# Optimization experiments

Hardware: AMD Instinct MI355X
Metric: run time of the kernel (lower is better)

## Reference

```python
import jax, jax.numpy as jnp
import numpy as np

EPS = 1e-6
POSE_W, DEPTH_W, POINTS_W, NORMAL_W = 1.0, 1.0, 1.0, 0.1
DEPTH_MIN = 1e-6


def mat_to_quat(M):
    # pytorch3d-style robust rotation-matrix -> quaternion (w,x,y,z)
    m00, m01, m02 = M[..., 0, 0], M[..., 0, 1], M[..., 0, 2]
    m10, m11, m12 = M[..., 1, 0], M[..., 1, 1], M[..., 1, 2]
    m20, m21, m22 = M[..., 2, 0], M[..., 2, 1], M[..., 2, 2]
    q_abs = jnp.sqrt(jnp.maximum(jnp.stack([
        1.0 + m00 + m11 + m22,
        1.0 + m00 - m11 - m22,
        1.0 - m00 + m11 - m22,
        1.0 - m00 - m11 + m22], axis=-1), 0.0))
    cand = jnp.stack([
        jnp.stack([q_abs[..., 0] ** 2, m21 - m12, m02 - m20, m10 - m01], -1),
        jnp.stack([m21 - m12, q_abs[..., 1] ** 2, m10 + m01, m02 + m20], -1),
        jnp.stack([m02 - m20, m10 + m01, q_abs[..., 2] ** 2, m12 + m21], -1),
        jnp.stack([m10 - m01, m20 + m02, m21 + m12, q_abs[..., 3] ** 2], -1),
    ], axis=-2)  # [...,4,4]
    cand = cand / (2.0 * jnp.maximum(q_abs[..., None], 0.1))
    best = jnp.argmax(q_abs, axis=-1)
    quat = jnp.take_along_axis(cand, best[..., None, None], axis=-2)[..., 0, :]
    return jnp.where(quat[..., 0:1] < 0, -quat, quat)


def pose_encoding(extri, intr, H, W):
    # extri [B,S,3,4] -> [B,S,9] = absT(3) + quat(4) + fov_h,fov_w
    T = extri[..., :3, 3]
    quat = mat_to_quat(extri[..., :3, :3])
    fov_h = 2.0 * jnp.arctan((H / 2.0) / intr[..., 1, 1])
    fov_w = 2.0 * jnp.arctan((W / 2.0) / intr[..., 0, 0])
    return jnp.concatenate([T, quat, fov_h[..., None], fov_w[..., None]], axis=-1)


def align_depth_scale(dp, dg, vm):
    # batched masked-median scale; dp detached by caller. Returns (aligned_gt, scales[B,S])
    B, S, H, W = dg.shape
    dpf, dgf = dp.reshape(B, S, H * W), dg.reshape(B, S, H * W)
    m = vm.reshape(B, S, H * W)
    m2 = m & jnp.isfinite(dpf) & (dpf > EPS)
    ratio = dpf / jnp.maximum(dgf, EPS)
    fm = m2 & jnp.isfinite(ratio)
    msum = m2.sum(-1)
    fcnt = fm.sum(-1)
    r = jnp.sort(jnp.where(fm, ratio, jnp.inf), axis=-1)
    idx = jnp.maximum((fcnt - 1) // 2, 0)  # torch lower median
    med = jnp.take_along_axis(r, idx[..., None], axis=-1)[..., 0]
    scale = jnp.clip(med, 1e-3, 1e3)
    scale = jnp.where((msum < 16) | (fcnt == 0), jnp.ones_like(scale), scale)
    return dg * scale[..., None, None], scale


def _cam_grid(depth, intr):
    B, S, H, W = depth.shape
    ys, xs = jnp.meshgrid(jnp.arange(H, dtype=depth.dtype),
                          jnp.arange(W, dtype=depth.dtype), indexing='ij')
    fx = intr[..., 0, 0][..., None, None]
    fy = intr[..., 1, 1][..., None, None]
    cx = intr[..., 0, 2][..., None, None]
    cy = intr[..., 1, 2][..., None, None]
    x = (xs - cx) / jnp.maximum(fx, EPS) * depth
    y = (ys - cy) / jnp.maximum(fy, EPS) * depth
    return jnp.stack([x, y, depth], axis=-1)  # [B,S,H,W,3]


def depth_to_normals(depth, intr):
    pts = _cam_grid(depth, intr)
    fx_diff = pts[..., 1:-1, 2:, :] - pts[..., 1:-1, :-2, :]
    fy_diff = pts[..., 2:, 1:-1, :] - pts[..., :-2, 1:-1, :]
    core = jnp.cross(fy_diff, fx_diff)
    core = core / jnp.maximum(jnp.linalg.norm(core, axis=-1, keepdims=True), EPS)
    return jnp.zeros_like(pts).at[..., 1:-1, 1:-1, :].set(core)


def depth_to_world_points(depth, intr, pose):
    cam_pts = _cam_grid(depth, intr)
    rot = pose[..., :3, :3]
    trans = pose[..., :3, 3]
    return jnp.einsum('bsij,bshwj->bshwi', rot, cam_pts) + trans[..., None, None, :]


def masked_l1(pred, target, mask):
    mask = mask.astype(pred.dtype)
    return ((pred - target) * mask).__abs__().sum() / jnp.maximum(mask.sum(), 1.0)


def masked_cosine_loss(pred, target, mask):
    pred = pred / jnp.maximum(jnp.linalg.norm(pred, axis=-1, keepdims=True), EPS)
    target = target / jnp.maximum(jnp.linalg.norm(target, axis=-1, keepdims=True), EPS)
    cos = jnp.clip((pred * target).sum(-1), -1.0, 1.0)
    m = mask.astype(cos.dtype)
    return ((1.0 - cos) * m).sum() / jnp.maximum(m.sum(), 1.0)


def smooth_l1(pred, target):
    d = jnp.abs(pred - target)
    return jnp.mean(jnp.where(d < 1.0, 0.5 * d * d, d - 0.5))


def supervised_loss(depth_pred, points_pred, pose_pred, depth_gt, intrinsics,
                    pose_matrix_gt, valid_mask):
    B, S, H, W = depth_gt.shape
    vm = valid_mask & jnp.isfinite(depth_gt) & (depth_gt > DEPTH_MIN)
    depth_gt_aligned, scales = align_depth_scale(
        jax.lax.stop_gradient(depth_pred), depth_gt, vm)
    points_gt = depth_to_world_points(depth_gt_aligned, intrinsics, pose_matrix_gt)
    points_mask = jnp.broadcast_to(vm[..., None], points_gt.shape)
    # normal mask: zero-out 1-pixel border
    border = jnp.zeros((H, W), dtype=bool).at[1:-1, 1:-1].set(True)
    normal_mask = vm & border
    pred_normals = depth_to_normals(depth_pred, intrinsics)
    gt_normals = depth_to_normals(depth_gt, intrinsics)
    normal_loss = masked_cosine_loss(pred_normals, gt_normals, normal_mask)
    pose_gt = pose_encoding(pose_matrix_gt[..., :3, :], intrinsics, H, W)
    pose_gt = pose_gt.at[..., :3].multiply(scales[..., None])
    depth_loss = masked_l1(depth_pred, depth_gt_aligned, vm)
    points_loss = masked_l1(points_pred, points_gt, points_mask)
    pose_loss = smooth_l1(pose_pred, pose_gt)
    return (POSE_W * pose_loss + DEPTH_W * depth_loss
            + POINTS_W * points_loss + NORMAL_W * normal_loss)


def setup_inputs() -> dict:
    key = jax.random.key(0)
    ks = jax.random.split(key, 7)
    B, S, H, W = 4, 8, 384, 512
    depth_gt = jax.random.uniform(ks[0], (B, S, H, W), minval=0.5, maxval=10.0)
    depth_pred = depth_gt * jax.random.uniform(ks[1], (B, S, H, W), minval=0.8, maxval=1.2)
    points_pred = jax.random.normal(ks[2], (B, S, H, W, 3))
    pose_pred = 0.1 * jax.random.normal(ks[3], (B, S, 9))
    intr = jnp.broadcast_to(jnp.array([[500.0, 0.0, W / 2.0],
                                       [0.0, 500.0, H / 2.0],
                                       [0.0, 0.0, 1.0]], jnp.float32), (B, S, 3, 3))
    q, _ = jnp.linalg.qr(jax.random.normal(ks[4], (B, S, 3, 3)))
    R = q * jnp.sign(jnp.linalg.det(q))[..., None, None]  # det=+1
    t = jax.random.normal(ks[5], (B, S, 3))
    top = jnp.concatenate([R, t[..., None]], axis=-1)
    bottom = jnp.broadcast_to(jnp.array([0.0, 0.0, 0.0, 1.0], jnp.float32), (B, S, 1, 4))
    pose_matrix_gt = jnp.concatenate([top, bottom], axis=-2)
    valid_mask = jax.random.uniform(ks[6], (B, S, H, W)) > 0.05
    return {"depth_pred": depth_pred, "points_pred": points_pred,
            "pose_pred": pose_pred, "depth_gt": depth_gt,
            "intrinsics": intr, "pose_matrix_gt": pose_matrix_gt,
            "valid_mask": valid_mask}


def reference(depth_pred, points_pred, pose_pred, depth_gt, intrinsics,
              pose_matrix_gt, valid_mask):
    return supervised_loss(depth_pred, points_pred, pose_pred, depth_gt,
                           intrinsics, pose_matrix_gt, valid_mask)
```

## Files before the change

### kernel.cpp

```cpp
#include <hip/hip_runtime.h>
#include <stdint.h>

#define H_ 384
#define W_ 512
#define HW_ (H_ * W_)
#define NIMG 32
#define EPSF 1e-6f
#define HBLK 16
#define HTHR 512
#define PXB (HW_ / HBLK)
#define CITER (PXB / (HTHR * 4))
#define MBLK 96
#define NPARTS (MBLK * NIMG)
#define SENT 0xFFFFFFFFu

#define OFF_MSUM   0
#define OFF_FCNT   32
#define OFF_KREM1  64
#define OFF_PREF1  96
#define OFF_POSE   128
#define OFF_PMF    160
#define OFF_PART   1184
#define OFF_PHA    16544
#define OFF_PHB    (OFF_PHA + NIMG*HBLK*2048)

__device__ __forceinline__ bool finitef(float x) {
    return ((__float_as_uint(x) >> 23) & 0xFFu) != 0xFFu;
}

__global__ __launch_bounds__(HTHR) void hist0_k(
    const float* __restrict__ dp, const float* __restrict__ dg,
    const uint8_t* __restrict__ vmask, uint32_t* __restrict__ ws)
{
    __shared__ uint32_t lh[2048];
    __shared__ int sm[8], sf[8];
    const int img = blockIdx.y, blk = blockIdx.x, t = threadIdx.x;
    for (int b = t; b < 2048; b += HTHR) lh[b] = 0;
    __syncthreads();

    const size_t base = (size_t)img * HW_;
    const float* dpi = dp + base;
    const float* dgi = dg + base;
    const uint8_t* mi = vmask + base;

    int m2c = 0, fmc = 0;

    for (int c = 0; c < CITER; ++c) {
        const int pix = blk * PXB + c * (HTHR * 4) + t * 4;
        const float4 v_dp = *reinterpret_cast<const float4*>(dpi + pix);
        const float4 v_dg = *reinterpret_cast<const float4*>(dgi + pix);
        const uchar4 v_m  = *reinterpret_cast<const uchar4*>(mi + pix);
        const float dpa[4] = {v_dp.x, v_dp.y, v_dp.z, v_dp.w};
        const float dga[4] = {v_dg.x, v_dg.y, v_dg.z, v_dg.w};
        const uint8_t ma[4] = {v_m.x, v_m.y, v_m.z, v_m.w};
        int bins[4]; bool fms[4];
#pragma unroll
        for (int e = 0; e < 4; ++e) {
            const float dgv = dga[e], dpv = dpa[e];
            const bool vm = ma[e] && finitef(dgv) && (dgv > 1e-6f);
            const bool m2 = vm && finitef(dpv) && (dpv > EPSF);
            const float ratio = dpv / fmaxf(dgv, EPSF);
            const bool fm = m2 && finitef(ratio);
            m2c += (int)m2; fmc += (int)fm;
            const uint32_t key = fm ? __float_as_uint(ratio) : SENT;
            bins[e] = (int)(key >> 21);
            fms[e] = fm;
        }

#pragma unroll
        for (int e = 0; e < 4; ++e) {
            const bool fm = fms[e];
            const int bin = bins[e];
            unsigned long long todo = __ballot(fm);
            while (todo) {
                const int lead = (int)__ffsll(todo) - 1;
                const int lbin = __shfl(bin, lead);
                const unsigned long long same = __ballot(fm && (bin == lbin));
                if ((t & 63) == lead)
                    atomicAdd(&lh[lbin], (uint32_t)__popcll(same));
                todo &= ~same;
            }
        }
    }

    for (int o = 32; o > 0; o >>= 1) { m2c += __shfl_down(m2c, o); fmc += __shfl_down(fmc, o); }
    if ((t & 63) == 0) { sm[t >> 6] = m2c; sf[t >> 6] = fmc; }
    __syncthreads();
    if (t == 0) {
        int M = 0, F = 0;
        for (int w = 0; w < 8; ++w) { M += sm[w]; F += sf[w]; }
        int* pmf = (int*)(ws + OFF_PMF) + (img * HBLK + blk) * 2;
        pmf[0] = M; pmf[1] = F;
    }

    uint32_t* phb = ws + OFF_PHA + (size_t)(img * HBLK + blk) * 2048;
    for (int b = t; b < 2048; b += HTHR) phb[b] = lh[b];
}

__global__ __launch_bounds__(HTHR) void histp1_k(
    const float* __restrict__ dp, const float* __restrict__ dg,
    const uint8_t* __restrict__ vmask, uint32_t* __restrict__ ws)
{
    __shared__ uint32_t lh[256];
    __shared__ uint32_t wsum[8];
    __shared__ int s_bin, s_krem, s_msum, s_fcnt;
    const int img = blockIdx.y, blk = blockIdx.x, t = threadIdx.x;

    const uint32_t* pin = ws + OFF_PHA + (size_t)img * HBLK * 2048;
    uint32_t local[4];
#pragma unroll
    for (int c = 0; c < 4; ++c) local[c] = 0;
    for (int b = 0; b < HBLK; ++b) {
        const uint32_t* row = pin + b * 2048 + t * 4;
#pragma unroll
        for (int c = 0; c < 4; ++c) local[c] += row[c];
    }
    const uint32_t cs = local[0] + local[1] + local[2] + local[3];

    uint32_t v = cs;
#pragma unroll
    for (int o = 1; o < 64; o <<= 1) {
        const uint32_t u = __shfl_up(v, o);
        if ((t & 63) >= o) v += u;
    }
    if ((t & 63) == 63) wsum[t >> 6] = v;
    if (t == 0) {
        s_bin = 0; s_krem = 0;
        const int* pmf = (const int*)(ws + OFF_PMF) + img * HBLK * 2;
        int M = 0, F = 0;
        for (int b = 0; b < HBLK; ++b) { M += pmf[2 * b]; F += pmf[2 * b + 1]; }
        s_msum = M; s_fcnt = F;
    }
    __syncthreads();
    uint32_t woff = 0;
    for (int w = 0; w < (t >> 6); ++w) woff += wsum[w];
    const uint32_t incl = woff + v;
    const uint32_t excl = incl - cs;

    const uint32_t k = (uint32_t)max((s_fcnt - 1) / 2, 0);
    if (k >= excl && k < incl) {
        uint32_t cum = excl;
#pragma unroll
        for (int c = 0; c < 4; ++c) {
            if (cum + local[c] > k) { s_bin = t * 4 + c; s_krem = (int)(k - cum); break; }
            cum += local[c];
        }
    }
    __syncthreads();
    if (t == 0 && blk == 0) {
        ((int*)(ws + OFF_MSUM))[img] = s_msum;
        ((int*)(ws + OFF_FCNT))[img] = s_fcnt;
        (ws + OFF_PREF1)[img] = (uint32_t)s_bin << 21;
        ((int*)(ws + OFF_KREM1))[img] = s_krem;
    }
    const uint32_t pm = (uint32_t)s_bin;

    if (t < 256) lh[t] = 0;
    __syncthreads();

    const size_t base = (size_t)img * HW_;
    for (int c = 0; c < CITER; ++c) {
        const int pix = blk * PXB + c * (HTHR * 4) + t * 4;
        const float4 v_dp = *reinterpret_cast<const float4*>(dp + base + pix);
        const float4 v_dg = *reinterpret_cast<const float4*>(dg + base + pix);
        const uchar4 v_m  = *reinterpret_cast<const uchar4*>(vmask + base + pix);
        const float dpa[4] = {v_dp.x, v_dp.y, v_dp.z, v_dp.w};
        const float dga[4] = {v_dg.x, v_dg.y, v_dg.z, v_dg.w};
        const uint8_t ma[4] = {v_m.x, v_m.y, v_m.z, v_m.w};
#pragma unroll
        for (int e = 0; e < 4; ++e) {
            const float dgv = dga[e], dpv = dpa[e];
            const bool vm = ma[e] && finitef(dgv) && (dgv > 1e-6f);
            const bool m2 = vm && finitef(dpv) && (dpv > EPSF);
            const float ratio = dpv / fmaxf(dgv, EPSF);
            const bool fm = m2 && finitef(ratio);
            const uint32_t key = fm ? __float_as_uint(ratio) : SENT;
            if ((key >> 21) == pm)
                atomicAdd(&lh[(key >> 13) & 255u], 1u);
        }
    }
    __syncthreads();

    uint32_t* pout = ws + OFF_PHB + (size_t)(img * HBLK + blk) * 256;
    if (t < 256) pout[t] = lh[t];
}

__global__ __launch_bounds__(256) void main_loss(
    const float* __restrict__ dp, const float* __restrict__ dg,
    const uint8_t* __restrict__ vmask, const float* __restrict__ pts_pred,
    const float* __restrict__ intr, const float* __restrict__ posegt,
    const float* __restrict__ posepred, uint32_t* __restrict__ ws)
{
    const int img = blockIdx.y;
    const int t = threadIdx.x;

    __shared__ uint32_t wsum[4];
    __shared__ int s_bin;
    __shared__ float sP[17];
    {
        const uint32_t* ph = ws + OFF_PHB + (size_t)img * HBLK * 256;
        uint32_t cs = 0;
        for (int b = 0; b < HBLK; ++b) cs += ph[b * 256 + t];
        uint32_t v = cs;
#pragma unroll
        for (int o = 1; o < 64; o <<= 1) {
            const uint32_t u = __shfl_up(v, o);
            if ((t & 63) >= o) v += u;
        }
        if ((t & 63) == 63) wsum[t >> 6] = v;
        if (t == 0) s_bin = 0;
        __syncthreads();
        uint32_t woff = 0;
        for (int w = 0; w < (t >> 6); ++w) woff += wsum[w];
        const uint32_t incl = woff + v;
        const uint32_t excl = incl - cs;
        const uint32_t k = (uint32_t)((const int*)(ws + OFF_KREM1))[img];
        if (k >= excl && k < incl) s_bin = t;
        __syncthreads();
    }
    if (t == 0) {
        const uint32_t med_u = (ws + OFF_PREF1)[img] | ((uint32_t)s_bin << 13) | 4096u;
        const float med = __uint_as_float(med_u);
        float sc_ = fminf(fmaxf(med, 0.001f), 1000.0f);
        const int fcnt = ((const int*)(ws + OFF_FCNT))[img];
        const int msum = ((const int*)(ws + OFF_MSUM))[img];
        if (msum < 16 || fcnt == 0) sc_ = 1.0f;

        const float* p = posegt + img * 16;
        sP[0] = p[0]; sP[1] = p[1]; sP[2] = p[2];  sP[9]  = p[3];
        sP[3] = p[4]; sP[4] = p[5]; sP[5] = p[6];  sP[10] = p[7];
        sP[6] = p[8]; sP[7] = p[9]; sP[8] = p[10]; sP[11] = p[11];
        sP[12] = intr[img * 9 + 0]; sP[13] = intr[img * 9 + 4];
        sP[14] = intr[img * 9 + 2]; sP[15] = intr[img * 9 + 5];
        sP[16] = sc_;

        if (blockIdx.x == 0) {
            const float m00 = p[0], m01 = p[1], m02 = p[2], tx = p[3];
            const float m10 = p[4], m11 = p[5], m12 = p[6], ty = p[7];
            const float m20 = p[8], m21 = p[9], m22 = p[10], tz = p[11];
            float qa[4];
            qa[0] = sqrtf(fmaxf(1.0f + m00 + m11 + m22, 0.0f));
            qa[1] = sqrtf(fmaxf(1.0f + m00 - m11 - m22, 0.0f));
            qa[2] = sqrtf(fmaxf(1.0f - m00 + m11 - m22, 0.0f));
            qa[3] = sqrtf(fmaxf(1.0f - m00 - m11 + m22, 0.0f));
            int best = 0; float bv = qa[0];
            for (int i2 = 1; i2 < 4; ++i2) if (qa[i2] > bv) { bv = qa[i2]; best = i2; }
            float c0, c1, c2, c3;
            if (best == 0)      { c0 = qa[0]*qa[0]; c1 = m21 - m12;   c2 = m02 - m20;   c3 = m10 - m01; }
            else if (best == 1) { c0 = m21 - m12;   c1 = qa[1]*qa[1]; c2 = m10 + m01;   c3 = m02 + m20; }
            else if (best == 2) { c0 = m02 - m20;   c1 = m10 + m01;   c2 = qa[2]*qa[2]; c3 = m12 + m21; }
            else                { c0 = m10 - m01;   c1 = m20 + m02;   c2 = m21 + m12;   c3 = qa[3]*qa[3]; }
            const float denom = 2.0f * fmaxf(qa[best], 0.1f);
            float q0 = c0 / denom, q1 = c1 / denom, q2 = c2 / denom, q3 = c3 / denom;
            if (q0 < 0.0f) { q0 = -q0; q1 = -q1; q2 = -q2; q3 = -q3; }
            const float fx = sP[12], fy = sP[13];
            const float fovh = 2.0f * atanf((H_ * 0.5f) / fy);
            const float fovw = 2.0f * atanf((W_ * 0.5f) / fx);
            const float pg[9] = {tx * sc_, ty * sc_, tz * sc_, q0, q1, q2, q3, fovh, fovw};
            const float* ppred = posepred + img * 9;
            float s = 0.0f;
            for (int i2 = 0; i2 < 9; ++i2) {
                const float d = fabsf(ppred[i2] - pg[i2]);
                s += (d < 1.0f) ? 0.5f * d * d : d - 0.5f;
            }
            ((float*)(ws + OFF_POSE))[img] = s;
        }
    }
    __syncthreads();
    const float R00 = sP[0], R01 = sP[1], R02 = sP[2];
    const float R10 = sP[3], R11 = sP[4], R12 = sP[5];
    const float R20 = sP[6], R21 = sP[7], R22 = sP[8];
    const float T0 = sP[9], T1 = sP[10], T2 = sP[11];
    const float inv_fx = 1.0f / fmaxf(sP[12], EPSF);
    const float inv_fy = 1.0f / fmaxf(sP[13], EPSF);
    const float cx = sP[14], cy = sP[15];
    const float sc = sP[16];

    const size_t base = (size_t)img * HW_;
    const int pix0 = (blockIdx.x * 256 + t) * 8;
    const int i = pix0 >> 9;
    const int j0 = pix0 & 511;
    const float* dpi = dp + base;
    const float* dgi = dg + base;

    const float4 dpC0 = *reinterpret_cast<const float4*>(dpi + pix0);
    const float4 dpC1 = *reinterpret_cast<const float4*>(dpi + pix0 + 4);
    const float4 dgC0 = *reinterpret_cast<const float4*>(dgi + pix0);
    const float4 dgC1 = *reinterpret_cast<const float4*>(dgi + pix0 + 4);
    const uchar4 m0 = *reinterpret_cast<const uchar4*>(vmask + base + pix0);
    const uchar4 m1 = *reinterpret_cast<const uchar4*>(vmask + base + pix0 + 4);
    const float4 pp0 = *reinterpret_cast<const float4*>(pts_pred + (base + pix0) * 3);
    const float4 pp1 = *reinterpret_cast<const float4*>(pts_pred + (base + pix0) * 3 + 4);
    const float4 pp2 = *reinterpret_cast<const float4*>(pts_pred + (base + pix0) * 3 + 8);
    const float4 pp3 = *reinterpret_cast<const float4*>(pts_pred + (base + pix0) * 3 + 12);
    const float4 pp4 = *reinterpret_cast<const float4*>(pts_pred + (base + pix0) * 3 + 16);
    const float4 pp5 = *reinterpret_cast<const float4*>(pts_pred + (base + pix0) * 3 + 20);

    const int im = (i > 0) ? i - 1 : 0;
    const int ip = (i < H_ - 1) ? i + 1 : i;
    const int jme = (j0 > 0) ? j0 - 1 : 0;
    const int jpe = (j0 + 8 < W_) ? j0 + 8 : W_ - 1;
    const float4 dpU0 = *reinterpret_cast<const float4*>(dpi + im * W_ + j0);
    const float4 dpU1 = *reinterpret_cast<const float4*>(dpi + im * W_ + j0 + 4);
    const float4 dpD0 = *reinterpret_cast<const float4*>(dpi + ip * W_ + j0);
    const float4 dpD1 = *reinterpret_cast<const float4*>(dpi + ip * W_ + j0 + 4);
    const float4 dgU0 = *reinterpret_cast<const float4*>(dgi + im * W_ + j0);
    const float4 dgU1 = *reinterpret_cast<const float4*>(dgi + im * W_ + j0 + 4);
    const float4 dgD0 = *reinterpret_cast<const float4*>(dgi + ip * W_ + j0);
    const float4 dgD1 = *reinterpret_cast<const float4*>(dgi + ip * W_ + j0 + 4);
    const float dpLe = dpi[i * W_ + jme], dpRe = dpi[i * W_ + jpe];
    const float dgLe = dgi[i * W_ + jme], dgRe = dgi[i * W_ + jpe];

    const float ppv[24] = {pp0.x, pp0.y, pp0.z, pp0.w, pp1.x, pp1.y, pp1.z, pp1.w,
                           pp2.x, pp2.y, pp2.z, pp2.w, pp3.x, pp3.y, pp3.z, pp3.w,
                           pp4.x, pp4.y, pp4.z, pp4.w, pp5.x, pp5.y, pp5.z, pp5.w};
    const float dpa[8] = {dpC0.x, dpC0.y, dpC0.z, dpC0.w, dpC1.x, dpC1.y, dpC1.z, dpC1.w};
    const float dga[8] = {dgC0.x, dgC0.y, dgC0.z, dgC0.w, dgC1.x, dgC1.y, dgC1.z, dgC1.w};
    const float dpUa[8] = {dpU0.x, dpU0.y, dpU0.z, dpU0.w, dpU1.x, dpU1.y, dpU1.z, dpU1.w};
    const float dpDa[8] = {dpD0.x, dpD0.y, dpD0.z, dpD0.w, dpD1.x, dpD1.y, dpD1.z, dpD1.w};
    const float dgUa[8] = {dgU0.x, dgU0.y, dgU0.z, dgU0.w, dgU1.x, dgU1.y, dgU1.z, dgU1.w};
    const float dgDa[8] = {dgD0.x, dgD0.y, dgD0.z, dgD0.w, dgD1.x, dgD1.y, dgD1.z, dgD1.w};
    const uint8_t ma[8] = {m0.x, m0.y, m0.z, m0.w, m1.x, m1.y, m1.z, m1.w};

    const float ay = ((float)i - cy) * inv_fy;
    const bool row_int = (i >= 1) && (i <= H_ - 2);

    float dsum = 0.0f, psum = 0.0f, nsum = 0.0f;
    float vcnt = 0.0f, ncnt = 0.0f;

#pragma unroll
    for (int e = 0; e < 8; ++e) {
        const int j = j0 + e;
        const float dgv = dga[e], dpv = dpa[e];
        const bool vm = ma[e] && finitef(dgv) && (dgv > 1e-6f);
        const bool nm = vm && row_int && (j >= 1) && (j <= W_ - 2);
        vcnt += vm ? 1.0f : 0.0f;
        ncnt += nm ? 1.0f : 0.0f;

        const float dal = dgv * sc;
        dsum += vm ? fabsf(dpv - dal) : 0.0f;
        const float ax = ((float)j - cx) * inv_fx;
        const float cxx = ax * dal, cyy = ay * dal;
        const float wx = R00 * cxx + R01 * cyy + R02 * dal + T0;
        const float wy = R10 * cxx + R11 * cyy + R12 * dal + T1;
        const float wz = R20 * cxx + R21 * cyy + R22 * dal + T2;
        const float pl = fabsf(ppv[3 * e] - wx) + fabsf(ppv[3 * e + 1] - wy)
                       + fabsf(ppv[3 * e + 2] - wz);
        psum += vm ? pl : 0.0f;

        const float pdL = (e == 0) ? dpLe : dpa[e - 1];
        const float pdR = (e == 7) ? dpRe : dpa[e + 1];
        const float gdL = (e == 0) ? dgLe : dga[e - 1];
        const float gdR = (e == 7) ? dgRe : dga[e + 1];
        const float pdU = dpUa[e], pdD = dpDa[e];
        const float gdU = dgUa[e], gdD = dgDa[e];

        const float dRLp = pdR - pdL, dDUp = pdD - pdU;
        const float Ap = inv_fy * (pdD + pdU);
        const float Bp = inv_fx * (pdR + pdL);
        const float cpx = dRLp * Ap;
        const float cpy = dDUp * Bp;
        const float cpz = -(Ap * Bp + ax * cpx + ay * cpy);
        const float dRLg = gdR - gdL, dDUg = gdD - gdU;
        const float Ag = inv_fy * (gdD + gdU);
        const float Bg = inv_fx * (gdR + gdL);
        const float cgx = dRLg * Ag;
        const float cgy = dDUg * Bg;
        const float cgz = -(Ag * Bg + ax * cgx + ay * cgy);

        const float np2 = cpx * cpx + cpy * cpy + cpz * cpz;
        const float ng2 = cgx * cgx + cgy * cgy + cgz * cgz;
        const float dpg = cpx * cgx + cpy * cgy + cpz * cgz;
        const float den = fmaxf(np2, 1e-12f) * fmaxf(ng2, 1e-12f);
        float cosv = dpg * __builtin_amdgcn_rsqf(den);
        cosv = fminf(fmaxf(cosv, -1.0f), 1.0f);
        nsum += nm ? (1.0f - cosv) : 0.0f;
    }

    float vals[5] = {vcnt, dsum, psum, nsum, ncnt};
    __shared__ float red[4][5];
    const int wave = t >> 6, lane = t & 63;
#pragma unroll
    for (int q = 0; q < 5; ++q) {
        float v = vals[q];
        for (int o = 32; o > 0; o >>= 1) v += __shfl_down(v, o);
        if (lane == 0) red[wave][q] = v;
    }
    __syncthreads();
    if (t == 0) {
        const int slot = blockIdx.y * gridDim.x + blockIdx.x;
        float* part = (float*)(ws + OFF_PART) + slot * 5;
#pragma unroll
        for (int q = 0; q < 5; ++q)
            part[q] = red[0][q] + red[1][q] + red[2][q] + red[3][q];
    }
}

__global__ __launch_bounds__(256) void finalize_k(const uint32_t* __restrict__ ws,
                                                  float* __restrict__ out)
{
    const float* part = (const float*)(ws + OFF_PART);
    const int t = threadIdx.x;
    double s[5] = {0, 0, 0, 0, 0};
    for (int slot = t; slot < NPARTS; slot += 256) {
#pragma unroll
        for (int q = 0; q < 5; ++q) s[q] += (double)part[slot * 5 + q];
    }
    __shared__ double red[4][5];
    const int wave = t >> 6, lane = t & 63;
#pragma unroll
    for (int q = 0; q < 5; ++q) {
        double v = s[q];
        for (int o = 32; o > 0; o >>= 1) v += __shfl_down(v, o);
        if (lane == 0) red[wave][q] = v;
    }
    __syncthreads();
    if (t == 0) {
        double tot[5];
#pragma unroll
        for (int q = 0; q < 5; ++q)
            tot[q] = red[0][q] + red[1][q] + red[2][q] + red[3][q];
        const float* pose = (const float*)(ws + OFF_POSE);
        double ps = 0.0;
        for (int i2 = 0; i2 < NIMG; ++i2) ps += (double)pose[i2];
        const double vmc = tot[0];
        const double depth_loss  = tot[1] / fmax(vmc, 1.0);
        const double points_loss = tot[2] / fmax(3.0 * vmc, 1.0);
        const double normal_loss = tot[3] / fmax(tot[4], 1.0);
        const double pose_loss   = ps / 288.0;
        out[0] = (float)(pose_loss + depth_loss + points_loss + 0.1 * normal_loss);
    }
}

extern "C" void kernel_launch(void* const* d_in, const int* in_sizes, int n_in,
                              void* d_out, int out_size, void* d_ws, size_t ws_size,
                              hipStream_t stream)
{
    const float*   dp       = (const float*)d_in[0];
    const float*   pts_pred = (const float*)d_in[1];
    const float*   posepred = (const float*)d_in[2];
    const float*   dg       = (const float*)d_in[3];
    const float*   intr     = (const float*)d_in[4];
    const float*   posegt   = (const float*)d_in[5];
    const uint8_t* vmask    = (const uint8_t*)d_in[6];
    float* out = (float*)d_out;
    uint32_t* ws = (uint32_t*)d_ws;

    const dim3 hgrid(HBLK, NIMG);
    hist0_k<<<hgrid, HTHR, 0, stream>>>(dp, dg, vmask, ws);
    histp1_k<<<hgrid, HTHR, 0, stream>>>(dp, dg, vmask, ws);
    main_loss<<<dim3(MBLK, NIMG), 256, 0, stream>>>(dp, dg, vmask, pts_pred, intr, posegt,
                                                     posepred, ws);
    finalize_k<<<1, 256, 0, stream>>>(ws, out);
}
```

Measured before the change: 68.64 us.

## Stage depth rows in shared memory tile and overlap loads with median scan

The main loss kernel now has each block handle two image rows. It cooperatively loads four rows of predicted and ground-truth depth (two rows plus halos) into shared memory, instead of each thread fetching its up, down and edge neighbors from global memory. Global loads are issued before the histogram scan, and one barrier is removed, so memory latency overlaps with finding the median bin. The thread that owns the median bin now writes the scale directly. Each thread processes 4 pixels instead of 8 and the grid is doubled, which trades fewer redundant loads and more parallelism for extra per-block prologue work (the histogram scan is repeated in twice as many blocks).

Result: slower. 70.15 us (+2.2%).

```diff
diff --git a/kernel.cpp b/kernel.cpp
--- a/kernel.cpp
+++ b/kernel.cpp
@@ -10,7 +10,7 @@
 #define HTHR 512
 #define PXB (HW_ / HBLK)
 #define CITER (PXB / (HTHR * 4))
-#define MBLK 96
+#define MBLK 192
 #define NPARTS (MBLK * NIMG)
 #define SENT 0xFFFFFFFFu
 
@@ -21,7 +21,7 @@
 #define OFF_POSE   128
 #define OFF_PMF    160
 #define OFF_PART   1184
-#define OFF_PHA    16544
+#define OFF_PHA    31904
 #define OFF_PHB    (OFF_PHA + NIMG*HBLK*2048)
 
 __device__ __forceinline__ bool finitef(float x) {
@@ -193,13 +193,39 @@
 {
     const int img = blockIdx.y;
     const int t = threadIdx.x;
-
+    const int i0 = blockIdx.x * 2;
+
+    __shared__ __align__(16) float tile[2][4][512];
     __shared__ uint32_t wsum[4];
-    __shared__ int s_bin;
     __shared__ float sP[17];
+
+    const size_t base = (size_t)img * HW_;
+    const float* dpi = dp + base;
+    const float* dgi = dg + base;
+
+    float4 stg[4];
+#pragma unroll
+    for (int q = 0; q < 4; ++q) {
+        const int idx = q * 256 + t;
+        const int arr = idx >> 9;
+        const int r   = (idx >> 7) & 3;
+        const int c4  = idx & 127;
+        int gr = i0 - 1 + r;
+        gr = gr < 0 ? 0 : (gr > H_ - 1 ? H_ - 1 : gr);
+        const float* src = arr ? dgi : dpi;
+        stg[q] = *reinterpret_cast<const float4*>(src + gr * W_ + c4 * 4);
+    }
+
+    const int pix0 = blockIdx.x * 1024 + t * 4;
+    const uchar4 v_m = *reinterpret_cast<const uchar4*>(vmask + base + pix0);
+    const float4 pp0 = *reinterpret_cast<const float4*>(pts_pred + (base + pix0) * 3);
+    const float4 pp1 = *reinterpret_cast<const float4*>(pts_pred + (base + pix0) * 3 + 4);
+    const float4 pp2 = *reinterpret_cast<const float4*>(pts_pred + (base + pix0) * 3 + 8);
+
+    uint32_t cs, vscan;
     {
         const uint32_t* ph = ws + OFF_PHB + (size_t)img * HBLK * 256;
-        uint32_t cs = 0;
+        cs = 0;
         for (int b = 0; b < HBLK; ++b) cs += ph[b * 256 + t];
         uint32_t v = cs;
 #pragma unroll
@@ -207,66 +233,41 @@
             const uint32_t u = __shfl_up(v, o);
             if ((t & 63) >= o) v += u;
         }
+        vscan = v;
         if ((t & 63) == 63) wsum[t >> 6] = v;
-        if (t == 0) s_bin = 0;
-        __syncthreads();
-        uint32_t woff = 0;
-        for (int w = 0; w < (t >> 6); ++w) woff += wsum[w];
-        const uint32_t incl = woff + v;
-        const uint32_t excl = incl - cs;
-        const uint32_t k = (uint32_t)((const int*)(ws + OFF_KREM1))[img];
-        if (k >= excl && k < incl) s_bin = t;
-        __syncthreads();
     }
     if (t == 0) {
-        const uint32_t med_u = (ws + OFF_PREF1)[img] | ((uint32_t)s_bin << 13) | 4096u;
-        const float med = __uint_as_float(med_u);
-        float sc_ = fminf(fmaxf(med, 0.001f), 1000.0f);
-        const int fcnt = ((const int*)(ws + OFF_FCNT))[img];
-        const int msum = ((const int*)(ws + OFF_MSUM))[img];
-        if (msum < 16 || fcnt == 0) sc_ = 1.0f;
-
         const float* p = posegt + img * 16;
         sP[0] = p[0]; sP[1] = p[1]; sP[2] = p[2];  sP[9]  = p[3];
         sP[3] = p[4]; sP[4] = p[5]; sP[5] = p[6];  sP[10] = p[7];
         sP[6] = p[8]; sP[7] = p[9]; sP[8] = p[10]; sP[11] = p[11];
         sP[12] = intr[img * 9 + 0]; sP[13] = intr[img * 9 + 4];
         sP[14] = intr[img * 9 + 2]; sP[15] = intr[img * 9 + 5];
-        sP[16] = sc_;
-
-        if (blockIdx.x == 0) {
-            const float m00 = p[0], m01 = p[1], m02 = p[2], tx = p[3];
-            const float m10 = p[4], m11 = p[5], m12 = p[6], ty = p[7];
-            const float m20 = p[8], m21 = p[9], m22 = p[10], tz = p[11];
-            float qa[4];
-            qa[0] = sqrtf(fmaxf(1.0f + m00 + m11 + m22, 0.0f));
-            qa[1] = sqrtf(fmaxf(1.0f + m00 - m11 - m22, 0.0f));
-            qa[2] = sqrtf(fmaxf(1.0f - m00 + m11 - m22, 0.0f));
-            qa[3] = sqrtf(fmaxf(1.0f - m00 - m11 + m22, 0.0f));
-            int best = 0; float bv = qa[0];
-            for (int i2 = 1; i2 < 4; ++i2) if (qa[i2] > bv) { bv = qa[i2]; best = i2; }
-            float c0, c1, c2, c3;
-            if (best == 0)      { c0 = qa[0]*qa[0]; c1 = m21 - m12;   c2 = m02 - m20;   c3 = m10 - m01; }
-            else if (best == 1) { c0 = m21 - m12;   c1 = qa[1]*qa[1]; c2 = m10 + m01;   c3 = m02 + m20; }
-            else if (best == 2) { c0 = m02 - m20;   c1 = m10 + m01;   c2 = qa[2]*qa[2]; c3 = m12 + m21; }
-            else                { c0 = m10 - m01;   c1 = m20 + m02;   c2 = m21 + m12;   c3 = qa[3]*qa[3]; }
-            const float denom = 2.0f * fmaxf(qa[best], 0.1f);
-            float q0 = c0 / denom, q1 = c1 / denom, q2 = c2 / denom, q3 = c3 / denom;
-            if (q0 < 0.0f) { q0 = -q0; q1 = -q1; q2 = -q2; q3 = -q3; }
-            const float fx = sP[12], fy = sP[13];
-            const float fovh = 2.0f * atanf((H_ * 0.5f) / fy);
-            const float fovw = 2.0f * atanf((W_ * 0.5f) / fx);
-            const float pg[9] = {tx * sc_, ty * sc_, tz * sc_, q0, q1, q2, q3, fovh, fovw};
-            const float* ppred = posepred + img * 9;
-            float s = 0.0f;
-            for (int i2 = 0; i2 < 9; ++i2) {
-                const float d = fabsf(ppred[i2] - pg[i2]);
-                s += (d < 1.0f) ? 0.5f * d * d : d - 0.5f;
-            }
-            ((float*)(ws + OFF_POSE))[img] = s;
-        }
-    }
-    __syncthreads();
+        sP[16] = 1.0f;
+    }
+
+    float4* tf4 = reinterpret_cast<float4*>(&tile[0][0][0]);
+#pragma unroll
+    for (int q = 0; q < 4; ++q) tf4[q * 256 + t] = stg[q];
+    __syncthreads();
+
+    {
+        uint32_t woff = 0;
+        for (int w = 0; w < (t >> 6); ++w) woff += wsum[w];
+        const uint32_t incl = woff + vscan;
+        const uint32_t excl = incl - cs;
+        const uint32_t k = (uint32_t)((const int*)(ws + OFF_KREM1))[img];
+        if (k >= excl && k < incl) {
+            const uint32_t med_u = (ws + OFF_PREF1)[img] | ((uint32_t)t << 13) | 4096u;
+            float sc_ = fminf(fmaxf(__uint_as_float(med_u), 0.001f), 1000.0f);
+            const int fcnt = ((const int*)(ws + OFF_FCNT))[img];
+            const int msum = ((const int*)(ws + OFF_MSUM))[img];
+            if (msum < 16 || fcnt == 0) sc_ = 1.0f;
+            sP[16] = sc_;
+        }
+    }
+    __syncthreads();
+
     const float R00 = sP[0], R01 = sP[1], R02 = sP[2];
     const float R10 = sP[3], R11 = sP[4], R12 = sP[5];
     const float R20 = sP[6], R21 = sP[7], R22 = sP[8];
@@ -276,51 +277,67 @@
     const float cx = sP[14], cy = sP[15];
     const float sc = sP[16];
 
-    const size_t base = (size_t)img * HW_;
-    const int pix0 = (blockIdx.x * 256 + t) * 8;
-    const int i = pix0 >> 9;
-    const int j0 = pix0 & 511;
-    const float* dpi = dp + base;
-    const float* dgi = dg + base;
-
-    const float4 dpC0 = *reinterpret_cast<const float4*>(dpi + pix0);
-    const float4 dpC1 = *reinterpret_cast<const float4*>(dpi + pix0 + 4);
-    const float4 dgC0 = *reinterpret_cast<const float4*>(dgi + pix0);
-    const float4 dgC1 = *reinterpret_cast<const float4*>(dgi + pix0 + 4);
-    const uchar4 m0 = *reinterpret_cast<const uchar4*>(vmask + base + pix0);
-    const uchar4 m1 = *reinterpret_cast<const uchar4*>(vmask + base + pix0 + 4);
-    const float4 pp0 = *reinterpret_cast<const float4*>(pts_pred + (base + pix0) * 3);
-    const float4 pp1 = *reinterpret_cast<const float4*>(pts_pred + (base + pix0) * 3 + 4);
-    const float4 pp2 = *reinterpret_cast<const float4*>(pts_pred + (base + pix0) * 3 + 8);
-    const float4 pp3 = *reinterpret_cast<const float4*>(pts_pred + (base + pix0) * 3 + 12);
-    const float4 pp4 = *reinterpret_cast<const float4*>(pts_pred + (base + pix0) * 3 + 16);
-    const float4 pp5 = *reinterpret_cast<const float4*>(pts_pred + (base + pix0) * 3 + 20);
-
-    const int im = (i > 0) ? i - 1 : 0;
-    const int ip = (i < H_ - 1) ? i + 1 : i;
+    if (blockIdx.x == 0 && t == 0) {
+        const float m00 = R00, m01 = R01, m02 = R02;
+        const float m10 = R10, m11 = R11, m12 = R12;
+        const float m20 = R20, m21 = R21, m22 = R22;
+        float qa[4];
+        qa[0] = sqrtf(fmaxf(1.0f + m00 + m11 + m22, 0.0f));
+        qa[1] = sqrtf(fmaxf(1.0f + m00 - m11 - m22, 0.0f));
+        qa[2] = sqrtf(fmaxf(1.0f - m00 + m11 - m22, 0.0f));
+        qa[3] = sqrtf(fmaxf(1.0f - m00 - m11 + m22, 0.0f));
+        int best = 0; float bv = qa[0];
+        for (int i2 = 1; i2 < 4; ++i2) if (qa[i2] > bv) { bv = qa[i2]; best = i2; }
+        float c0, c1, c2, c3;
+        if (best == 0)      { c0 = qa[0]*qa[0]; c1 = m21 - m12;   c2 = m02 - m20;   c3 = m10 - m01; }
+        else if (best == 1) { c0 = m21 - m12;   c1 = qa[1]*qa[1]; c2 = m10 + m01;   c3 = m02 + m20; }
+        else if (best == 2) { c0 = m02 - m20;   c1 = m10 + m01;   c2 = qa[2]*qa[2]; c3 = m12 + m21; }
+        else                { c0 = m10 - m01;   c1 = m20 + m02;   c2 = m21 + m12;   c3 = qa[3]*qa[3]; }
+        const float denom = 2.0f * fmaxf(qa[best], 0.1f);
+        float q0 = c0 / denom, q1 = c1 / denom, q2 = c2 / denom, q3 = c3 / denom;
+        if (q0 < 0.0f) { q0 = -q0; q1 = -q1; q2 = -q2; q3 = -q3; }
+        const float fovh = 2.0f * atanf((H_ * 0.5f) / sP[13]);
+        const float fovw = 2.0f * atanf((W_ * 0.5f) / sP[12]);
+        const float pg[9] = {T0 * sc, T1 * sc, T2 * sc, q0, q1, q2, q3, fovh, fovw};
+        const float* ppred = posepred + img * 9;
+        float s = 0.0f;
+        for (int i2 = 0; i2 < 9; ++i2) {
+            const float d = fabsf(ppred[i2] - pg[i2]);
+            s += (d < 1.0f) ? 0.5f * d * d : d - 0.5f;
+        }
+        ((float*)(ws + OFF_POSE))[img] = s;
+    }
+
+    const int lr = 1 + (t >> 7);
+    const int j0 = (t & 127) * 4;
+    const int i  = i0 + (t >> 7);
+    const float* tdpC = &tile[0][lr][0];
+    const float* tdpU = &tile[0][lr - 1][0];
+    const float* tdpD = &tile[0][lr + 1][0];
+    const float* tdgC = &tile[1][lr][0];
+    const float* tdgU = &tile[1][lr - 1][0];
+    const float* tdgD = &tile[1][lr + 1][0];
+
+    const float4 dpC = *reinterpret_cast<const float4*>(tdpC + j0);
+    const float4 dpU = *reinterpret_cast<const float4*>(tdpU + j0);
+    const float4 dpD = *reinterpret_cast<const float4*>(tdpD + j0);
+    const float4 dgC = *reinterpret_cast<const float4*>(tdgC + j0);
+    const float4 dgU = *reinterpret_cast<const float4*>(tdgU + j0);
+    const float4 dgD = *reinterpret_cast<const float4*>(tdgD + j0);
     const int jme = (j0 > 0) ? j0 - 1 : 0;
-    const int jpe = (j0 + 8 < W_) ? j0 + 8 : W_ - 1;
-    const float4 dpU0 = *reinterpret_cast<const float4*>(dpi + im * W_ + j0);
-    const float4 dpU1 = *reinterpret_cast<const float4*>(dpi + im * W_ + j0 + 4);
-    const float4 dpD0 = *reinterpret_cast<const float4*>(dpi + ip * W_ + j0);
-    const float4 dpD1 = *reinterpret_cast<const float4*>(dpi + ip * W_ + j0 + 4);
-    const float4 dgU0 = *reinterpret_cast<const float4*>(dgi + im * W_ + j0);
-    const float4 dgU1 = *reinterpret_cast<const float4*>(dgi + im * W_ + j0 + 4);
-    const float4 dgD0 = *reinterpret_cast<const float4*>(dgi + ip * W_ + j0);
-    const float4 dgD1 = *reinterpret_cast<const float4*>(dgi + ip * W_ + j0 + 4);
-    const float dpLe = dpi[i * W_ + jme], dpRe = dpi[i * W_ + jpe];
-    const float dgLe = dgi[i * W_ + jme], dgRe = dgi[i * W_ + jpe];
-
-    const float ppv[24] = {pp0.x, pp0.y, pp0.z, pp0.w, pp1.x, pp1.y, pp1.z, pp1.w,
-                           pp2.x, pp2.y, pp2.z, pp2.w, pp3.x, pp3.y, pp3.z, pp3.w,
-                           pp4.x, pp4.y, pp4.z, pp4.w, pp5.x, pp5.y, pp5.z, pp5.w};
-    const float dpa[8] = {dpC0.x, dpC0.y, dpC0.z, dpC0.w, dpC1.x, dpC1.y, dpC1.z, dpC1.w};
-    const float dga[8] = {dgC0.x, dgC0.y, dgC0.z, dgC0.w, dgC1.x, dgC1.y, dgC1.z, dgC1.w};
-    const float dpUa[8] = {dpU0.x, dpU0.y, dpU0.z, dpU0.w, dpU1.x, dpU1.y, dpU1.z, dpU1.w};
-    const float dpDa[8] = {dpD0.x, dpD0.y, dpD0.z, dpD0.w, dpD1.x, dpD1.y, dpD1.z, dpD1.w};
-    const float dgUa[8] = {dgU0.x, dgU0.y, dgU0.z, dgU0.w, dgU1.x, dgU1.y, dgU1.z, dgU1.w};
-    const float dgDa[8] = {dgD0.x, dgD0.y, dgD0.z, dgD0.w, dgD1.x, dgD1.y, dgD1.z, dgD1.w};
-    const uint8_t ma[8] = {m0.x, m0.y, m0.z, m0.w, m1.x, m1.y, m1.z, m1.w};
+    const int jpe = (j0 + 4 < W_) ? j0 + 4 : W_ - 1;
+    const float dpLe = tdpC[jme], dpRe = tdpC[jpe];
+    const float dgLe = tdgC[jme], dgRe = tdgC[jpe];
+
+    const float ppv[12] = {pp0.x, pp0.y, pp0.z, pp0.w, pp1.x, pp1.y, pp1.z, pp1.w,
+                           pp2.x, pp2.y, pp2.z, pp2.w};
+    const float dpa[4] = {dpC.x, dpC.y, dpC.z, dpC.w};
+    const float dga[4] = {dgC.x, dgC.y, dgC.z, dgC.w};
+    const float dpUa[4] = {dpU.x, dpU.y, dpU.z, dpU.w};
+    const float dpDa[4] = {dpD.x, dpD.y, dpD.z, dpD.w};
+    const float dgUa[4] = {dgU.x, dgU.y, dgU.z, dgU.w};
+    const float dgDa[4] = {dgD.x, dgD.y, dgD.z, dgD.w};
+    const uint8_t ma[4] = {v_m.x, v_m.y, v_m.z, v_m.w};
 
     const float ay = ((float)i - cy) * inv_fy;
     const bool row_int = (i >= 1) && (i <= H_ - 2);
@@ -329,7 +346,7 @@
     float vcnt = 0.0f, ncnt = 0.0f;
 
 #pragma unroll
-    for (int e = 0; e < 8; ++e) {
+    for (int e = 0; e < 4; ++e) {
         const int j = j0 + e;
         const float dgv = dga[e], dpv = dpa[e];
         const bool vm = ma[e] && finitef(dgv) && (dgv > 1e-6f);
@@ -349,9 +366,9 @@
         psum += vm ? pl : 0.0f;
 
         const float pdL = (e == 0) ? dpLe : dpa[e - 1];
-        const float pdR = (e == 7) ? dpRe : dpa[e + 1];
+        const float pdR = (e == 3) ? dpRe : dpa[e + 1];
         const float gdL = (e == 0) ? dgLe : dga[e - 1];
-        const float gdR = (e == 7) ? dgRe : dga[e + 1];
+        const float gdR = (e == 3) ? dgRe : dga[e + 1];
         const float pdU = dpUa[e], pdD = dpDa[e];
         const float gdU = dgUa[e], gdD = dgDa[e];
 
```

## Move normal-consistency loss into second histogram pass and prefetch main loads

Applied to the files above, without the earlier changes.

The surface-normal cosine loss, which does not depend on the median scale, is moved from main_loss into histp1_k, which already streams depth_pred and depth_gt for the same pixels. Per-block normal sums and counts go to a new workspace region that finalize_k reads. main_loss now issues its depth, mask and point loads before the histogram scan so global reads overlap the median-selection work, and it no longer loads neighbour rows. In exchange histp1_k does more loads and arithmetic per pixel and uses more registers, and it runs on only 16 blocks per image.

New measurement: 72.92 us. 1.06x slower.

```diff
diff --git a/kernel.cpp b/kernel.cpp
--- a/kernel.cpp
+++ b/kernel.cpp
@@ -20,8 +20,9 @@
 #define OFF_PREF1  96
 #define OFF_POSE   128
 #define OFF_PMF    160
-#define OFF_PART   1184
-#define OFF_PHA    16544
+#define OFF_PNC    1184
+#define OFF_PART   2208
+#define OFF_PHA    11424
 #define OFF_PHB    (OFF_PHA + NIMG*HBLK*2048)
 
 __device__ __forceinline__ bool finitef(float x) {
@@ -99,11 +100,14 @@
 
 __global__ __launch_bounds__(HTHR) void histp1_k(
     const float* __restrict__ dp, const float* __restrict__ dg,
-    const uint8_t* __restrict__ vmask, uint32_t* __restrict__ ws)
+    const uint8_t* __restrict__ vmask, const float* __restrict__ intr,
+    uint32_t* __restrict__ ws)
 {
     __shared__ uint32_t lh[256];
     __shared__ uint32_t wsum[8];
     __shared__ int s_bin, s_krem, s_msum, s_fcnt;
+    __shared__ float sI[4];
+    __shared__ float sns[8]; __shared__ int snc[8];
     const int img = blockIdx.y, blk = blockIdx.x, t = threadIdx.x;
 
     const uint32_t* pin = ws + OFF_PHA + (size_t)img * HBLK * 2048;
@@ -130,6 +134,10 @@
         int M = 0, F = 0;
         for (int b = 0; b < HBLK; ++b) { M += pmf[2 * b]; F += pmf[2 * b + 1]; }
         s_msum = M; s_fcnt = F;
+        sI[0] = 1.0f / fmaxf(intr[img * 9 + 0], EPSF);
+        sI[1] = 1.0f / fmaxf(intr[img * 9 + 4], EPSF);
+        sI[2] = intr[img * 9 + 2];
+        sI[3] = intr[img * 9 + 5];
     }
     __syncthreads();
     uint32_t woff = 0;
@@ -154,21 +162,49 @@
         ((int*)(ws + OFF_KREM1))[img] = s_krem;
     }
     const uint32_t pm = (uint32_t)s_bin;
+    const float inv_fx = sI[0], inv_fy = sI[1], cx = sI[2], cy = sI[3];
 
     if (t < 256) lh[t] = 0;
     __syncthreads();
 
     const size_t base = (size_t)img * HW_;
+    const float* dpi = dp + base;
+    const float* dgi = dg + base;
+    float nsum = 0.0f; int ncc = 0;
+
     for (int c = 0; c < CITER; ++c) {
         const int pix = blk * PXB + c * (HTHR * 4) + t * 4;
-        const float4 v_dp = *reinterpret_cast<const float4*>(dp + base + pix);
-        const float4 v_dg = *reinterpret_cast<const float4*>(dg + base + pix);
+        const int i = pix >> 9;
+        const int j0 = pix & 511;
+        const float4 v_dp = *reinterpret_cast<const float4*>(dpi + pix);
+        const float4 v_dg = *reinterpret_cast<const float4*>(dgi + pix);
         const uchar4 v_m  = *reinterpret_cast<const uchar4*>(vmask + base + pix);
+
+        const int im = (i > 0) ? i - 1 : 0;
+        const int ip = (i < H_ - 1) ? i + 1 : i;
+        const int jme = (j0 > 0) ? j0 - 1 : 0;
+        const int jpe = (j0 + 4 < W_) ? j0 + 4 : W_ - 1;
+        const float4 dpU = *reinterpret_cast<const float4*>(dpi + im * W_ + j0);
+        const float4 dpD = *reinterpret_cast<const float4*>(dpi + ip * W_ + j0);
+        const float4 dgU = *reinterpret_cast<const float4*>(dgi + im * W_ + j0);
+        const float4 dgD = *reinterpret_cast<const float4*>(dgi + ip * W_ + j0);
+        const float dpLe = dpi[i * W_ + jme], dpRe = dpi[i * W_ + jpe];
+        const float dgLe = dgi[i * W_ + jme], dgRe = dgi[i * W_ + jpe];
+
         const float dpa[4] = {v_dp.x, v_dp.y, v_dp.z, v_dp.w};
         const float dga[4] = {v_dg.x, v_dg.y, v_dg.z, v_dg.w};
+        const float dpUa[4] = {dpU.x, dpU.y, dpU.z, dpU.w};
+        const float dpDa[4] = {dpD.x, dpD.y, dpD.z, dpD.w};
+        const float dgUa[4] = {dgU.x, dgU.y, dgU.z, dgU.w};
+        const float dgDa[4] = {dgD.x, dgD.y, dgD.z, dgD.w};
         const uint8_t ma[4] = {v_m.x, v_m.y, v_m.z, v_m.w};
+
+        const float ay = ((float)i - cy) * inv_fy;
+        const bool row_int = (i >= 1) && (i <= H_ - 2);
+
 #pragma unroll
         for (int e = 0; e < 4; ++e) {
+            const int j = j0 + e;
             const float dgv = dga[e], dpv = dpa[e];
             const bool vm = ma[e] && finitef(dgv) && (dgv > 1e-6f);
             const bool m2 = vm && finitef(dpv) && (dpv > EPSF);
@@ -177,12 +213,53 @@
             const uint32_t key = fm ? __float_as_uint(ratio) : SENT;
             if ((key >> 21) == pm)
                 atomicAdd(&lh[(key >> 13) & 255u], 1u);
+
+            const bool nm = vm && row_int && (j >= 1) && (j <= W_ - 2);
+            const float pdL = (e == 0) ? dpLe : dpa[e - 1];
+            const float pdR = (e == 3) ? dpRe : dpa[e + 1];
+            const float gdL = (e == 0) ? dgLe : dga[e - 1];
+            const float gdR = (e == 3) ? dgRe : dga[e + 1];
+            const float pdU = dpUa[e], pdD = dpDa[e];
+            const float gdU = dgUa[e], gdD = dgDa[e];
+            const float ax = ((float)j - cx) * inv_fx;
+
+            const float dRLp = pdR - pdL, dDUp = pdD - pdU;
+            const float Ap = inv_fy * (pdD + pdU);
+            const float Bp = inv_fx * (pdR + pdL);
+            const float cpx = dRLp * Ap;
+            const float cpy = dDUp * Bp;
+            const float cpz = -(Ap * Bp + ax * cpx + ay * cpy);
+            const float dRLg = gdR - gdL, dDUg = gdD - gdU;
+            const float Ag = inv_fy * (gdD + gdU);
+            const float Bg = inv_fx * (gdR + gdL);
+            const float cgx = dRLg * Ag;
+            const float cgy = dDUg * Bg;
+            const float cgz = -(Ag * Bg + ax * cgx + ay * cgy);
+
+            const float np2 = cpx * cpx + cpy * cpy + cpz * cpz;
+            const float ng2 = cgx * cgx + cgy * cgy + cgz * cgz;
+            const float dpg = cpx * cgx + cpy * cgy + cpz * cgz;
+            const float den = fmaxf(np2, 1e-12f) * fmaxf(ng2, 1e-12f);
+            float cosv = dpg * __builtin_amdgcn_rsqf(den);
+            cosv = fminf(fmaxf(cosv, -1.0f), 1.0f);
+            nsum += nm ? (1.0f - cosv) : 0.0f;
+            ncc  += nm ? 1 : 0;
         }
     }
     __syncthreads();
 
     uint32_t* pout = ws + OFF_PHB + (size_t)(img * HBLK + blk) * 256;
     if (t < 256) pout[t] = lh[t];
+
+    for (int o = 32; o > 0; o >>= 1) { nsum += __shfl_down(nsum, o); ncc += __shfl_down(ncc, o); }
+    if ((t & 63) == 0) { sns[t >> 6] = nsum; snc[t >> 6] = ncc; }
+    __syncthreads();
+    if (t == 0) {
+        float NS = 0.0f; int NC = 0;
+        for (int w = 0; w < 8; ++w) { NS += sns[w]; NC += snc[w]; }
+        float* pnc = (float*)(ws + OFF_PNC) + (img * HBLK + blk) * 2;
+        pnc[0] = NS; pnc[1] = (float)NC;
+    }
 }
 
 __global__ __launch_bounds__(256) void main_loss(
@@ -193,6 +270,23 @@
 {
     const int img = blockIdx.y;
     const int t = threadIdx.x;
+
+    const size_t base = (size_t)img * HW_;
+    const int pix0 = (blockIdx.x * 256 + t) * 8;
+    const int i = pix0 >> 9;
+    const int j0 = pix0 & 511;
+    const float4 dpC0 = *reinterpret_cast<const float4*>(dp + base + pix0);
+    const float4 dpC1 = *reinterpret_cast<const float4*>(dp + base + pix0 + 4);
+    const float4 dgC0 = *reinterpret_cast<const float4*>(dg + base + pix0);
+    const float4 dgC1 = *reinterpret_cast<const float4*>(dg + base + pix0 + 4);
+    const uchar4 m0 = *reinterpret_cast<const uchar4*>(vmask + base + pix0);
+    const uchar4 m1 = *reinterpret_cast<const uchar4*>(vmask + base + pix0 + 4);
+    const float4 pp0 = *reinterpret_cast<const float4*>(pts_pred + (base + pix0) * 3);
+    const float4 pp1 = *reinterpret_cast<const float4*>(pts_pred + (base + pix0) * 3 + 4);
+    const float4 pp2 = *reinterpret_cast<const float4*>(pts_pred + (base + pix0) * 3 + 8);
+    const float4 pp3 = *reinterpret_cast<const float4*>(pts_pred + (base + pix0) * 3 + 12);
+    const float4 pp4 = *reinterpret_cast<const float4*>(pts_pred + (base + pix0) * 3 + 16);
+    const float4 pp5 = *reinterpret_cast<const float4*>(pts_pred + (base + pix0) * 3 + 20);
 
     __shared__ uint32_t wsum[4];
     __shared__ int s_bin;
@@ -220,8 +314,7 @@
     }
     if (t == 0) {
         const uint32_t med_u = (ws + OFF_PREF1)[img] | ((uint32_t)s_bin << 13) | 4096u;
-        const float med = __uint_as_float(med_u);
-        float sc_ = fminf(fmaxf(med, 0.001f), 1000.0f);
+        float sc_ = fminf(fmaxf(__uint_as_float(med_u), 0.001f), 1000.0f);
         const int fcnt = ((const int*)(ws + OFF_FCNT))[img];
         const int msum = ((const int*)(ws + OFF_MSUM))[img];
         if (msum < 16 || fcnt == 0) sc_ = 1.0f;
@@ -253,9 +346,8 @@
             const float denom = 2.0f * fmaxf(qa[best], 0.1f);
             float q0 = c0 / denom, q1 = c1 / denom, q2 = c2 / denom, q3 = c3 / denom;
             if (q0 < 0.0f) { q0 = -q0; q1 = -q1; q2 = -q2; q3 = -q3; }
-            const float fx = sP[12], fy = sP[13];
-            const float fovh = 2.0f * atanf((H_ * 0.5f) / fy);
-            const float fovw = 2.0f * atanf((W_ * 0.5f) / fx);
+            const float fovh = 2.0f * atanf((H_ * 0.5f) / sP[13]);
+            const float fovw = 2.0f * atanf((W_ * 0.5f) / sP[12]);
             const float pg[9] = {tx * sc_, ty * sc_, tz * sc_, q0, q1, q2, q3, fovh, fovw};
             const float* ppred = posepred + img * 9;
             float s = 0.0f;
@@ -276,67 +368,22 @@
     const float cx = sP[14], cy = sP[15];
     const float sc = sP[16];
 
-    const size_t base = (size_t)img * HW_;
-    const int pix0 = (blockIdx.x * 256 + t) * 8;
-    const int i = pix0 >> 9;
-    const int j0 = pix0 & 511;
-    const float* dpi = dp + base;
-    const float* dgi = dg + base;
-
-    const float4 dpC0 = *reinterpret_cast<const float4*>(dpi + pix0);
-    const float4 dpC1 = *reinterpret_cast<const float4*>(dpi + pix0 + 4);
-    const float4 dgC0 = *reinterpret_cast<const float4*>(dgi + pix0);
-    const float4 dgC1 = *reinterpret_cast<const float4*>(dgi + pix0 + 4);
-    const uchar4 m0 = *reinterpret_cast<const uchar4*>(vmask + base + pix0);
-    const uchar4 m1 = *reinterpret_cast<const uchar4*>(vmask + base + pix0 + 4);
-    const float4 pp0 = *reinterpret_cast<const float4*>(pts_pred + (base + pix0) * 3);
-    const float4 pp1 = *reinterpret_cast<const float4*>(pts_pred + (base + pix0) * 3 + 4);
-    const float4 pp2 = *reinterpret_cast<const float4*>(pts_pred + (base + pix0) * 3 + 8);
-    const float4 pp3 = *reinterpret_cast<const float4*>(pts_pred + (base + pix0) * 3 + 12);
-    const float4 pp4 = *reinterpret_cast<const float4*>(pts_pred + (base + pix0) * 3 + 16);
-    const float4 pp5 = *reinterpret_cast<const float4*>(pts_pred + (base + pix0) * 3 + 20);
-
-    const int im = (i > 0) ? i - 1 : 0;
-    const int ip = (i < H_ - 1) ? i + 1 : i;
-    const int jme = (j0 > 0) ? j0 - 1 : 0;
-    const int jpe = (j0 + 8 < W_) ? j0 + 8 : W_ - 1;
-    const float4 dpU0 = *reinterpret_cast<const float4*>(dpi + im * W_ + j0);
-    const float4 dpU1 = *reinterpret_cast<const float4*>(dpi + im * W_ + j0 + 4);
-    const float4 dpD0 = *reinterpret_cast<const float4*>(dpi + ip * W_ + j0);
-    const float4 dpD1 = *reinterpret_cast<const float4*>(dpi + ip * W_ + j0 + 4);
-    const float4 dgU0 = *reinterpret_cast<const float4*>(dgi + im * W_ + j0);
-    const float4 dgU1 = *reinterpret_cast<const float4*>(dgi + im * W_ + j0 + 4);
-    const float4 dgD0 = *reinterpret_cast<const float4*>(dgi + ip * W_ + j0);
-    const float4 dgD1 = *reinterpret_cast<const float4*>(dgi + ip * W_ + j0 + 4);
-    const float dpLe = dpi[i * W_ + jme], dpRe = dpi[i * W_ + jpe];
-    const float dgLe = dgi[i * W_ + jme], dgRe = dgi[i * W_ + jpe];
-
     const float ppv[24] = {pp0.x, pp0.y, pp0.z, pp0.w, pp1.x, pp1.y, pp1.z, pp1.w,
                            pp2.x, pp2.y, pp2.z, pp2.w, pp3.x, pp3.y, pp3.z, pp3.w,
                            pp4.x, pp4.y, pp4.z, pp4.w, pp5.x, pp5.y, pp5.z, pp5.w};
     const float dpa[8] = {dpC0.x, dpC0.y, dpC0.z, dpC0.w, dpC1.x, dpC1.y, dpC1.z, dpC1.w};
     const float dga[8] = {dgC0.x, dgC0.y, dgC0.z, dgC0.w, dgC1.x, dgC1.y, dgC1.z, dgC1.w};
-    const float dpUa[8] = {dpU0.x, dpU0.y, dpU0.z, dpU0.w, dpU1.x, dpU1.y, dpU1.z, dpU1.w};
-    const float dpDa[8] = {dpD0.x, dpD0.y, dpD0.z, dpD0.w, dpD1.x, dpD1.y, dpD1.z, dpD1.w};
-    const float dgUa[8] = {dgU0.x, dgU0.y, dgU0.z, dgU0.w, dgU1.x, dgU1.y, dgU1.z, dgU1.w};
-    const float dgDa[8] = {dgD0.x, dgD0.y, dgD0.z, dgD0.w, dgD1.x, dgD1.y, dgD1.z, dgD1.w};
     const uint8_t ma[8] = {m0.x, m0.y, m0.z, m0.w, m1.x, m1.y, m1.z, m1.w};
 
     const float ay = ((float)i - cy) * inv_fy;
-    const bool row_int = (i >= 1) && (i <= H_ - 2);
-
-    float dsum = 0.0f, psum = 0.0f, nsum = 0.0f;
-    float vcnt = 0.0f, ncnt = 0.0f;
-
+
+    float dsum = 0.0f, psum = 0.0f, vcnt = 0.0f;
 #pragma unroll
     for (int e = 0; e < 8; ++e) {
         const int j = j0 + e;
         const float dgv = dga[e], dpv = dpa[e];
         const bool vm = ma[e] && finitef(dgv) && (dgv > 1e-6f);
-        const bool nm = vm && row_int && (j >= 1) && (j <= W_ - 2);
         vcnt += vm ? 1.0f : 0.0f;
-        ncnt += nm ? 1.0f : 0.0f;
-
         const float dal = dgv * sc;
         dsum += vm ? fabsf(dpv - dal) : 0.0f;
         const float ax = ((float)j - cx) * inv_fx;
@@ -347,41 +394,13 @@
         const float pl = fabsf(ppv[3 * e] - wx) + fabsf(ppv[3 * e + 1] - wy)
                        + fabsf(ppv[3 * e + 2] - wz);
         psum += vm ? pl : 0.0f;
-
-        const float pdL = (e == 0) ? dpLe : dpa[e - 1];
-        const float pdR = (e == 7) ? dpRe : dpa[e + 1];
-        const float gdL = (e == 0) ? dgLe : dga[e - 1];
-        const float gdR = (e == 7) ? dgRe : dga[e + 1];
-        const float pdU = dpUa[e], pdD = dpDa[e];
-        const float gdU = dgUa[e], gdD = dgDa[e];
-
-        const float dRLp = pdR - pdL, dDUp = pdD - pdU;
-        const float Ap = inv_fy * (pdD + pdU);
-        const float Bp = inv_fx * (pdR + pdL);
-        const float cpx = dRLp * Ap;
-        const float cpy = dDUp * Bp;
-        const float cpz = -(Ap * Bp + ax * cpx + ay * cpy);
-        const float dRLg = gdR - gdL, dDUg = gdD - gdU;
-        const float Ag = inv_fy * (gdD + gdU);
-        const float Bg = inv_fx * (gdR + gdL);
-        const float cgx = dRLg * Ag;
-        const float cgy = dDUg * Bg;
-        const float cgz = -(Ag * Bg + ax * cgx + ay * cgy);
-
-        const float np2 = cpx * cpx + cpy * cpy + cpz * cpz;
-        const float ng2 = cgx * cgx + cgy * cgy + cgz * cgz;
-        const float dpg = cpx * cgx + cpy * cgy + cpz * cgz;
-        const float den = fmaxf(np2, 1e-12f) * fmaxf(ng2, 1e-12f);
-        float cosv = dpg * __builtin_amdgcn_rsqf(den);
-        cosv = fminf(fmaxf(cosv, -1.0f), 1.0f);
-        nsum += nm ? (1.0f - cosv) : 0.0f;
-    }
-
-    float vals[5] = {vcnt, dsum, psum, nsum, ncnt};
-    __shared__ float red[4][5];
+    }
+
+    float vals[3] = {vcnt, dsum, psum};
+    __shared__ float red[4][3];
     const int wave = t >> 6, lane = t & 63;
 #pragma unroll
-    for (int q = 0; q < 5; ++q) {
+    for (int q = 0; q < 3; ++q) {
         float v = vals[q];
         for (int o = 32; o > 0; o >>= 1) v += __shfl_down(v, o);
         if (lane == 0) red[wave][q] = v;
@@ -389,9 +408,9 @@
     __syncthreads();
     if (t == 0) {
         const int slot = blockIdx.y * gridDim.x + blockIdx.x;
-        float* part = (float*)(ws + OFF_PART) + slot * 5;
-#pragma unroll
-        for (int q = 0; q < 5; ++q)
+        float* part = (float*)(ws + OFF_PART) + slot * 3;
+#pragma unroll
+        for (int q = 0; q < 3; ++q)
             part[q] = red[0][q] + red[1][q] + red[2][q] + red[3][q];
     }
 }
@@ -401,16 +420,23 @@
 {
     const float* part = (const float*)(ws + OFF_PART);
     const int t = threadIdx.x;
-    double s[5] = {0, 0, 0, 0, 0};
+    double s0 = 0, s1 = 0, s2 = 0, sn = 0, sc2 = 0;
     for (int slot = t; slot < NPARTS; slot += 256) {
-#pragma unroll
-        for (int q = 0; q < 5; ++q) s[q] += (double)part[slot * 5 + q];
+        s0 += (double)part[slot * 3 + 0];
+        s1 += (double)part[slot * 3 + 1];
+        s2 += (double)part[slot * 3 + 2];
+    }
+    const float* pnc = (const float*)(ws + OFF_PNC);
+    for (int slot = t; slot < NIMG * HBLK; slot += 256) {
+        sn  += (double)pnc[slot * 2 + 0];
+        sc2 += (double)pnc[slot * 2 + 1];
     }
     __shared__ double red[4][5];
     const int wave = t >> 6, lane = t & 63;
+    double dv[5] = {s0, s1, s2, sn, sc2};
 #pragma unroll
     for (int q = 0; q < 5; ++q) {
-        double v = s[q];
+        double v = dv[q];
         for (int o = 32; o > 0; o >>= 1) v += __shfl_down(v, o);
         if (lane == 0) red[wave][q] = v;
     }
@@ -448,7 +474,7 @@
 
     const dim3 hgrid(HBLK, NIMG);
     hist0_k<<<hgrid, HTHR, 0, stream>>>(dp, dg, vmask, ws);
-    histp1_k<<<hgrid, HTHR, 0, stream>>>(dp, dg, vmask, ws);
+    histp1_k<<<hgrid, HTHR, 0, stream>>>(dp, dg, vmask, intr, ws);
     main_loss<<<dim3(MBLK, NIMG), 256, 0, stream>>>(dp, dg, vmask, pts_pred, intr, posegt,
                                                      posepred, ws);
     finalize_k<<<1, 256, 0, stream>>>(ws, out);
```
